# Kernel tuning notes

Measured on AMD Instinct MI355X. Metric: run time of the kernel, lower is better.

## Reference

```python
import jax, jax.numpy as jnp
import numpy as np

B = 4096
P_HID = 1024
H_HID = 512
MAX_P = 128
MAX_HE = MAX_P // 3  # 42
TAU = 1.0
EPS = 1e-20


def setup_inputs() -> dict:
    key = jax.random.key(0)
    ks = jax.random.split(key, 12)
    s_p = 1.0 / np.sqrt(P_HID)
    s_h = 1.0 / np.sqrt(H_HID)
    # gumbel noise: g = -log(-log(U))
    u_p = jax.random.uniform(ks[3], (B, MAX_P, 2), minval=EPS, maxval=1.0)
    u_h = jax.random.uniform(ks[4], (B, MAX_HE, 2), minval=EPS, maxval=1.0)
    return {
        "particle_h": jax.random.normal(ks[0], (B, P_HID), jnp.float32),
        "edge_h": jax.random.normal(ks[1], (B, H_HID), jnp.float32),
        "hyperedge_h": jax.random.normal(ks[2], (B, H_HID), jnp.float32),
        "g_p": -jnp.log(-jnp.log(u_p)),
        "g_h": -jnp.log(-jnp.log(u_h)),
        "W1_p": jax.random.normal(ks[5], (P_HID, P_HID), jnp.float32) * s_p,
        "b1_p": jnp.zeros((P_HID,), jnp.float32),
        "W2_p": jax.random.normal(ks[6], (P_HID, MAX_P), jnp.float32) * s_p,
        "b2_p": jnp.zeros((MAX_P,), jnp.float32),
        "W1_h": jax.random.normal(ks[7], (H_HID, H_HID), jnp.float32) * s_h,
        "b1_h": jnp.zeros((H_HID,), jnp.float32),
        "W2_h": jax.random.normal(ks[8], (H_HID, MAX_HE), jnp.float32) * s_h,
        "b2_h": jnp.zeros((MAX_HE,), jnp.float32),
    }


def _gumbel_hard_st(logits, g, tau):
    """F.gumbel_softmax(stack([l,-l],-1), tau, hard=True)[...,0] (straight-through)."""
    y = jax.nn.softmax((jnp.stack([logits, -logits], axis=-1) + g) / tau, axis=-1)
    y0 = y[..., 0]
    hard0 = (y0 > y[..., 1]).astype(y0.dtype)
    return hard0 + y0 - jax.lax.stop_gradient(y0)


def _mlp(x, W1, b1, W2, b2):
    return jax.nn.gelu(x @ W1 + b1, approximate=False) @ W2 + b2


def reference(particle_h, edge_h, hyperedge_h, g_p, g_h,
              W1_p, b1_p, W2_p, b2_p, W1_h, b1_h, W2_h, b2_h):
    particle_logits = _mlp(particle_h, W1_p, b1_p, W2_p, b2_p)      # [B, MAX_P]
    particle_mask = _gumbel_hard_st(particle_logits, g_p, TAU)      # [B, MAX_P]
    n_particles = particle_mask.sum(axis=-1).astype(jnp.int32)      # [B]

    # Ragged edge lists as a fixed padded buffer: all C(MAX_P,2) lexicographic
    # pairs (same order as torch.combinations); pair (i,j), i<j, is valid for
    # batch b iff j < n_particles[b].
    ii, jj = jnp.triu_indices(MAX_P, k=1)
    edge_index = jnp.stack([ii, jj]).astype(jnp.int32)              # [2, E_max]
    edge_valid = jj[None, :] < n_particles[:, None]                 # [B, E_max] bool

    hyperedge_logits = _mlp(hyperedge_h, W1_h, b1_h, W2_h, b2_h)    # [B, MAX_HE]
    hyperedge_mask = _gumbel_hard_st(hyperedge_logits, g_h, TAU)
    n_hyperedges = hyperedge_mask.sum(axis=-1).astype(jnp.int32)

    return (particle_mask, n_particles, edge_index, edge_valid,
            hyperedge_mask, n_hyperedges)
```

## Files before the change

### kernel.cpp

```cpp
#include <hip/hip_runtime.h>
#include <hip/hip_bf16.h>
#include <math.h>

typedef __bf16 bf16_t;
typedef bf16_t bf16x8 __attribute__((ext_vector_type(8)));
typedef bf16_t bf16x4 __attribute__((ext_vector_type(4)));
typedef float f32x4 __attribute__((ext_vector_type(4)));
typedef unsigned int u32;

#define B_SZ 4096
#define P_HID 1024
#define H_HID 512
#define MAX_P 128
#define MAX_HE 42
#define HE_PAD 64
#define E_MAX 8128
#define E_MAX4 2032

__device__ __forceinline__ void async_cp16(const bf16_t* g, bf16_t* l) {
    __builtin_amdgcn_global_load_lds(
        (const __attribute__((address_space(1))) u32*)g,
        (__attribute__((address_space(3))) u32*)l, 16, 0, 0);
}

__device__ __forceinline__ float gelu_exact(float v) {
    return 0.5f * v * (1.f + erff(v * 0.70710678118654752f));
}

template<int BM, int BN, int MODE>
__global__ __launch_bounds__(256, 2) void gemm_t(
    const bf16_t* __restrict__ Ahi, const bf16_t* __restrict__ Alo,
    const bf16_t* __restrict__ BThi, const bf16_t* __restrict__ BTlo,
    const float* __restrict__ bias,
    bf16_t* __restrict__ Chi, bf16_t* __restrict__ Clo, float* __restrict__ Cf,
    int N, int K, int kchunk)
{
    constexpr int MT = BM / 32;
    constexpr int NT = BN / 32;
    constexpr int OPS_A = BM / 16;
    constexpr int OPS_B = BN / 16;
    constexpr int NOPS = 2 * OPS_A + 2 * OPS_B;

    __shared__ __align__(16) bf16_t smem[(2 * BM + 2 * BN) * 32];
    bf16_t* const As0 = smem;
    bf16_t* const As1 = smem + BM * 32;
    bf16_t* const Bs0 = smem + 2 * BM * 32;
    bf16_t* const Bs1 = smem + 2 * BM * 32 + BN * 32;

    const int tid  = threadIdx.x;
    const int lane = tid & 63;
    const int wid  = tid >> 6;
    const int wm   = wid & 1;
    const int wn   = wid >> 1;
    const int bm   = blockIdx.y * BM;
    const int bn   = blockIdx.x * BN;
    const int k0   = blockIdx.z * kchunk;

    const int srow = lane >> 2;
    const int scol = (lane & 3) * 8;

    f32x4 acc[MT][NT];
#pragma unroll
    for (int i = 0; i < MT; ++i)
#pragma unroll
        for (int j = 0; j < NT; ++j)
            acc[i][j] = (f32x4){0.f, 0.f, 0.f, 0.f};

    const bf16_t* const gA0 = Ahi  + (size_t)bm * K;
    const bf16_t* const gA1 = Alo  + (size_t)bm * K;
    const bf16_t* const gB0 = BThi + (size_t)bn * K;
    const bf16_t* const gB1 = BTlo + (size_t)bn * K;

    const int fr = lane & 15;
    const int fq = lane >> 4;

    for (int kt = k0; kt < k0 + kchunk; kt += 32) {
        __syncthreads();
#pragma unroll
        for (int o = 0; o < NOPS; ++o) {
            if ((o & 3) != wid) continue;
            const bf16_t* gsrc;
            bf16_t* lbase;
            int q;
            if (o < OPS_A)                  { q = o;                     gsrc = gA0; lbase = As0; }
            else if (o < 2 * OPS_A)         { q = o - OPS_A;             gsrc = gA1; lbase = As1; }
            else if (o < 2 * OPS_A + OPS_B) { q = o - 2 * OPS_A;         gsrc = gB0; lbase = Bs0; }
            else                            { q = o - 2 * OPS_A - OPS_B; gsrc = gB1; lbase = Bs1; }
            async_cp16(gsrc + (size_t)(q * 16 + srow) * K + kt + scol,
                       lbase + q * 16 * 32);
        }
        __syncthreads();

        bf16x8 ah[MT], al[MT], bh[NT], bl[NT];
#pragma unroll
        for (int i = 0; i < MT; ++i) {
            const int row = wm * (BM / 2) + i * 16 + fr;
            ah[i] = *(const bf16x8*)(As0 + row * 32 + fq * 8);
            al[i] = *(const bf16x8*)(As1 + row * 32 + fq * 8);
        }
#pragma unroll
        for (int j = 0; j < NT; ++j) {
            const int row = wn * (BN / 2) + j * 16 + fr;
            bh[j] = *(const bf16x8*)(Bs0 + row * 32 + fq * 8);
            bl[j] = *(const bf16x8*)(Bs1 + row * 32 + fq * 8);
        }
#pragma unroll
        for (int i = 0; i < MT; ++i)
#pragma unroll
            for (int j = 0; j < NT; ++j) {
                acc[i][j] = __builtin_amdgcn_mfma_f32_16x16x32_bf16(ah[i], bh[j], acc[i][j], 0, 0, 0);
                acc[i][j] = __builtin_amdgcn_mfma_f32_16x16x32_bf16(ah[i], bl[j], acc[i][j], 0, 0, 0);
                acc[i][j] = __builtin_amdgcn_mfma_f32_16x16x32_bf16(al[i], bh[j], acc[i][j], 0, 0, 0);
            }
    }

#pragma unroll
    for (int i = 0; i < MT; ++i)
#pragma unroll
        for (int j = 0; j < NT; ++j) {
            const int col  = bn + wn * (BN / 2) + j * 16 + fr;
            const int row0 = bm + wm * (BM / 2) + i * 16 + fq * 4;
            if (MODE == 0) {
                const float bj = bias[col];
#pragma unroll
                for (int r = 0; r < 4; ++r) {
                    float v = gelu_exact(acc[i][j][r] + bj);
                    bf16_t h = (bf16_t)v;
                    bf16_t l = (bf16_t)(v - (float)h);
                    const size_t off = (size_t)(row0 + r) * N + col;
                    Chi[off] = h;
                    Clo[off] = l;
                }
            } else {
#pragma unroll
                for (int r = 0; r < 4; ++r)
                    atomicAdd(&Cf[(size_t)(row0 + r) * N + col], acc[i][j][r]);
            }
        }
}

struct PrepArgs {
    const float *ph, *hh, *W1p, *W2p, *W1h, *W2h, *b2p, *b2h;
    bf16_t *pA_hi, *pA_lo, *hA_hi, *hA_lo;
    bf16_t *W1pT_hi, *W1pT_lo, *W2pT_hi, *W2pT_lo;
    bf16_t *W1hT_hi, *W1hT_lo, *W2hT_hi, *W2hT_lo;
    float *log_p, *log_h;
    float *out_ei; int *ws_jj;
};

__device__ __forceinline__ void split4(const float* x, bf16_t* hi, bf16_t* lo, int i) {
    float4 v = ((const float4*)x)[i];
    float vv[4] = {v.x, v.y, v.z, v.w};
    bf16x4 h, l;
#pragma unroll
    for (int r = 0; r < 4; ++r) {
        bf16_t hh = (bf16_t)vv[r];
        h[r] = hh;
        l[r] = (bf16_t)(vv[r] - (float)hh);
    }
    ((bf16x4*)hi)[i] = h;
    ((bf16x4*)lo)[i] = l;
}

__device__ __forceinline__ void tsplit(
    const float* W, bf16_t* Thi, bf16_t* Tlo, int K, int N,
    int t, int nx, float (*sh)[33], int tid)
{
    const int n0 = (t % nx) * 32, k0 = (t / nx) * 32;
    const int tx = tid & 31, ty = tid >> 5;
    for (int r = ty; r < 32; r += 8) {
        const int n = n0 + tx;
        sh[r][tx] = (n < N) ? W[(size_t)(k0 + r) * N + n] : 0.f;
    }
    __syncthreads();
    for (int r = ty; r < 32; r += 8) {
        const float x = sh[tx][r];
        bf16_t h = (bf16_t)x;
        bf16_t l = (bf16_t)(x - (float)h);
        const size_t off = (size_t)(n0 + r) * K + k0 + tx;
        Thi[off] = h;
        Tlo[off] = l;
    }
}

__device__ __forceinline__ int tri_off(int i) { return (i * (255 - i)) >> 1; }

__global__ __launch_bounds__(256) void prep_all(PrepArgs a)
{
    __shared__ float sh[32][33];
    const int bid = blockIdx.x;
    const int tid = threadIdx.x;

    if (bid < 4096) {
        split4(a.ph, a.pA_hi, a.pA_lo, bid * 256 + tid);
    } else if (bid < 6144) {
        split4(a.hh, a.hA_hi, a.hA_lo, (bid - 4096) * 256 + tid);
    } else if (bid < 7168) {
        tsplit(a.W1p, a.W1pT_hi, a.W1pT_lo, P_HID, P_HID, bid - 6144, 32, sh, tid);
    } else if (bid < 7296) {
        tsplit(a.W2p, a.W2pT_hi, a.W2pT_lo, P_HID, MAX_P, bid - 7168, 4, sh, tid);
    } else if (bid < 7552) {
        tsplit(a.W1h, a.W1hT_hi, a.W1hT_lo, H_HID, H_HID, bid - 7296, 16, sh, tid);
    } else if (bid < 7584) {
        tsplit(a.W2h, a.W2hT_hi, a.W2hT_lo, H_HID, MAX_HE, bid - 7552, 2, sh, tid);
    } else if (bid < 7616) {
        const int e = (bid - 7584) * 256 + tid;
        if (e < E_MAX) {
            int i = (int)((255.0 - sqrt(65025.0 - 8.0 * (double)e)) * 0.5);
            if (i < 0) i = 0;
            if (i > 126) i = 126;
            while (i > 0 && tri_off(i) > e) --i;
            while (i < 126 && tri_off(i + 1) <= e) ++i;
            const int j = i + 1 + (e - tri_off(i));
            a.out_ei[e] = (float)i;
            a.out_ei[E_MAX + e] = (float)j;
            a.ws_jj[e] = j;
        }
    } else if (bid < 9664) {
        const int i = (bid - 7616) * 256 + tid;
        a.log_p[i] = a.b2p[i & (MAX_P - 1)];
    } else {
        const int i = (bid - 9664) * 256 + tid;
        const int c = i & (HE_PAD - 1);
        a.log_h[i] = (c < MAX_HE) ? a.b2h[c] : 0.f;
    }
}

__global__ __launch_bounds__(256) void mask_both(
    const float* __restrict__ log_p, const float* __restrict__ g_p,
    const float* __restrict__ log_h, const float* __restrict__ g_h,
    float* __restrict__ out_pmask, float* __restrict__ out_np, int* __restrict__ ws_np,
    float* __restrict__ out_hmask, float* __restrict__ out_nh)
{
    const int gw   = blockIdx.x * 4 + (threadIdx.x >> 6);
    const int lane = threadIdx.x & 63;
    float c = 0.f;
    if (gw < B_SZ) {
        const int row = gw;
#pragma unroll
        for (int h = 0; h < 2; ++h) {
            const int i = lane + 64 * h;
            const size_t idx = (size_t)row * MAX_P + i;
            const float l  = log_p[idx];
            const float g0 = g_p[2 * idx + 0];
            const float g1 = g_p[2 * idx + 1];
            const float m = ((l + g0) > (g1 - l)) ? 1.f : 0.f;
            out_pmask[idx] = m;
            c += m;
        }
#pragma unroll
        for (int off = 32; off > 0; off >>= 1) c += __shfl_xor(c, off, 64);
        if (lane == 0) { out_np[row] = c; ws_np[row] = (int)c; }
    } else {
        const int row = gw - B_SZ;
        if (lane < MAX_HE) {
            const size_t idx = (size_t)row * MAX_HE + lane;
            const float l  = log_h[(size_t)row * HE_PAD + lane];
            const float g0 = g_h[2 * idx + 0];
            const float g1 = g_h[2 * idx + 1];
            const float m = ((l + g0) > (g1 - l)) ? 1.f : 0.f;
            out_hmask[idx] = m;
            c = m;
        }
#pragma unroll
        for (int off = 32; off > 0; off >>= 1) c += __shfl_xor(c, off, 64);
        if (lane == 0) out_nh[row] = c;
    }
}

__global__ __launch_bounds__(256) void edge_valid_kernel(
    const int* __restrict__ ws_jj, const int* __restrict__ ws_n,
    float* __restrict__ out)
{
    const int b   = blockIdx.x >> 1;
    const int seg = blockIdx.x & 1;
    const int n   = ws_n[b];
    const int base = seg * (E_MAX4 / 2);
    float* const orow = out + (size_t)b * E_MAX;
#pragma unroll
    for (int it = 0; it < 4; ++it) {
        const int q = base + it * 256 + threadIdx.x;
        if (q < base + E_MAX4 / 2) {
            const int4 j4 = ((const int4*)ws_jj)[q];
            float4 v;
            v.x = (j4.x < n) ? 1.f : 0.f;
            v.y = (j4.y < n) ? 1.f : 0.f;
            v.z = (j4.z < n) ? 1.f : 0.f;
            v.w = (j4.w < n) ? 1.f : 0.f;
            ((float4*)orow)[q] = v;
        }
    }
}

extern "C" void kernel_launch(void* const* d_in, const int* in_sizes, int n_in,
                              void* d_out, int out_size, void* d_ws, size_t ws_size,
                              hipStream_t stream)
{
    const float* particle_h  = (const float*)d_in[0];
    const float* hyperedge_h = (const float*)d_in[2];
    const float* g_p  = (const float*)d_in[3];
    const float* g_h  = (const float*)d_in[4];
    const float* W1_p = (const float*)d_in[5];
    const float* b1_p = (const float*)d_in[6];
    const float* W2_p = (const float*)d_in[7];
    const float* b2_p = (const float*)d_in[8];
    const float* W1_h = (const float*)d_in[9];
    const float* b1_h = (const float*)d_in[10];
    const float* W2_h = (const float*)d_in[11];
    const float* b2_h = (const float*)d_in[12];

    float* out = (float*)d_out;
    float* out_pmask = out;
    float* out_np    = out_pmask + (size_t)B_SZ * MAX_P;
    float* out_ei    = out_np + B_SZ;
    float* out_ev    = out_ei + 2 * E_MAX;
    float* out_hmask = out_ev + (size_t)B_SZ * E_MAX;
    float* out_nh    = out_hmask + (size_t)B_SZ * MAX_HE;

    char* w = (char*)d_ws;
    bf16_t* pA_hi   = (bf16_t*)w;  w += (size_t)B_SZ * P_HID * 2;
    bf16_t* pA_lo   = (bf16_t*)w;  w += (size_t)B_SZ * P_HID * 2;
    bf16_t* hA_hi   = (bf16_t*)w;  w += (size_t)B_SZ * H_HID * 2;
    bf16_t* hA_lo   = (bf16_t*)w;  w += (size_t)B_SZ * H_HID * 2;
    bf16_t* hidp_hi = (bf16_t*)w;  w += (size_t)B_SZ * P_HID * 2;
    bf16_t* hidp_lo = (bf16_t*)w;  w += (size_t)B_SZ * P_HID * 2;
    bf16_t* hidh_hi = (bf16_t*)w;  w += (size_t)B_SZ * H_HID * 2;
    bf16_t* hidh_lo = (bf16_t*)w;  w += (size_t)B_SZ * H_HID * 2;
    bf16_t* W1pT_hi = (bf16_t*)w;  w += (size_t)P_HID * P_HID * 2;
    bf16_t* W1pT_lo = (bf16_t*)w;  w += (size_t)P_HID * P_HID * 2;
    bf16_t* W2pT_hi = (bf16_t*)w;  w += (size_t)MAX_P * P_HID * 2;
    bf16_t* W2pT_lo = (bf16_t*)w;  w += (size_t)MAX_P * P_HID * 2;
    bf16_t* W1hT_hi = (bf16_t*)w;  w += (size_t)H_HID * H_HID * 2;
    bf16_t* W1hT_lo = (bf16_t*)w;  w += (size_t)H_HID * H_HID * 2;
    bf16_t* W2hT_hi = (bf16_t*)w;  w += (size_t)HE_PAD * H_HID * 2;
    bf16_t* W2hT_lo = (bf16_t*)w;  w += (size_t)HE_PAD * H_HID * 2;
    float*  log_p   = (float*)w;   w += (size_t)B_SZ * MAX_P * 4;
    float*  log_h   = (float*)w;   w += (size_t)B_SZ * HE_PAD * 4;
    int*    ws_np   = (int*)w;     w += B_SZ * 4;
    int*    ws_jj   = (int*)w;

    PrepArgs pa;
    pa.ph = particle_h; pa.hh = hyperedge_h;
    pa.W1p = W1_p; pa.W2p = W2_p; pa.W1h = W1_h; pa.W2h = W2_h;
    pa.b2p = b2_p; pa.b2h = b2_h;
    pa.pA_hi = pA_hi; pa.pA_lo = pA_lo; pa.hA_hi = hA_hi; pa.hA_lo = hA_lo;
    pa.W1pT_hi = W1pT_hi; pa.W1pT_lo = W1pT_lo;
    pa.W2pT_hi = W2pT_hi; pa.W2pT_lo = W2pT_lo;
    pa.W1hT_hi = W1hT_hi; pa.W1hT_lo = W1hT_lo;
    pa.W2hT_hi = W2hT_hi; pa.W2hT_lo = W2hT_lo;
    pa.log_p = log_p; pa.log_h = log_h;
    pa.out_ei = out_ei; pa.ws_jj = ws_jj;
    prep_all<<<10688, 256, 0, stream>>>(pa);

    gemm_t<128, 128, 0><<<dim3(P_HID / 128, B_SZ / 128), 256, 0, stream>>>(
        pA_hi, pA_lo, W1pT_hi, W1pT_lo, b1_p, hidp_hi, hidp_lo, nullptr,
        P_HID, P_HID, P_HID);
    gemm_t<128, 64, 0><<<dim3(H_HID / 64, B_SZ / 128), 256, 0, stream>>>(
        hA_hi, hA_lo, W1hT_hi, W1hT_lo, b1_h, hidh_hi, hidh_lo, nullptr,
        H_HID, H_HID, H_HID);

    gemm_t<128, 128, 1><<<dim3(1, B_SZ / 128, 4), 256, 0, stream>>>(
        hidp_hi, hidp_lo, W2pT_hi, W2pT_lo, nullptr, nullptr, nullptr, log_p,
        MAX_P, P_HID, P_HID / 4);
    gemm_t<128, 64, 1><<<dim3(1, B_SZ / 128, 4), 256, 0, stream>>>(
        hidh_hi, hidh_lo, W2hT_hi, W2hT_lo, nullptr, nullptr, nullptr, log_h,
        HE_PAD, H_HID, H_HID / 4);

    mask_both<<<2 * B_SZ / 4, 256, 0, stream>>>(
        log_p, g_p, log_h, g_h, out_pmask, out_np, ws_np, out_hmask, out_nh);

    edge_valid_kernel<<<2 * B_SZ, 256, 0, stream>>>(ws_jj, ws_np, out_ev);
}
```

Measured before the change: 316.8 us.

## Fuse gumbel mask into second GEMM, load B directly from global, retile

The second-layer GEMMs now apply bias, the Gumbel hard threshold and the per-row count in their epilogue. This removes the split-K atomics, the logits buffers, their bias initialisation in prep, and the separate mask kernel. The B operand is now read straight from global/L2 into registers instead of being staged in LDS. Tile shapes also change: first-layer tiles go to 64x128 and the split-K grids are dropped, so the second layer runs fewer, longer blocks with less parallelism.

```diff
diff --git a/kernel.cpp b/kernel.cpp
--- a/kernel.cpp
+++ b/kernel.cpp
@@ -27,38 +27,38 @@
     return 0.5f * v * (1.f + erff(v * 0.70710678118654752f));
 }
 
-template<int BM, int BN, int MODE>
-__global__ __launch_bounds__(256, 2) void gemm_t(
+template<int BM, int BN, int WM, int WN, int MODE>
+__global__ __launch_bounds__(256, 2) void gemm_f(
     const bf16_t* __restrict__ Ahi, const bf16_t* __restrict__ Alo,
     const bf16_t* __restrict__ BThi, const bf16_t* __restrict__ BTlo,
     const float* __restrict__ bias,
-    bf16_t* __restrict__ Chi, bf16_t* __restrict__ Clo, float* __restrict__ Cf,
-    int N, int K, int kchunk)
-{
-    constexpr int MT = BM / 32;
-    constexpr int NT = BN / 32;
-    constexpr int OPS_A = BM / 16;
-    constexpr int OPS_B = BN / 16;
-    constexpr int NOPS = 2 * OPS_A + 2 * OPS_B;
-
-    __shared__ __align__(16) bf16_t smem[(2 * BM + 2 * BN) * 32];
-    bf16_t* const As0 = smem;
-    bf16_t* const As1 = smem + BM * 32;
-    bf16_t* const Bs0 = smem + 2 * BM * 32;
-    bf16_t* const Bs1 = smem + 2 * BM * 32 + BN * 32;
+    bf16_t* __restrict__ Chi, bf16_t* __restrict__ Clo,
+    int N, int K,
+    const float* __restrict__ g, float* __restrict__ out_mask,
+    float* __restrict__ out_n, int* __restrict__ ws_n, int NV)
+{
+    constexpr int MT = BM / (WM * 16);
+    constexpr int NT = BN / (WN * 16);
+    constexpr int AOPS = BM / 16;
+
+    __shared__ __align__(16) bf16_t As0[BM * 32];
+    __shared__ __align__(16) bf16_t As1[BM * 32];
+    __shared__ float cnt[BM][WN];
 
     const int tid  = threadIdx.x;
     const int lane = tid & 63;
     const int wid  = tid >> 6;
-    const int wm   = wid & 1;
-    const int wn   = wid >> 1;
+    const int wm   = wid % WM;
+    const int wn   = wid / WM;
     const int bm   = blockIdx.y * BM;
     const int bn   = blockIdx.x * BN;
-    const int k0   = blockIdx.z * kchunk;
 
     const int srow = lane >> 2;
     const int scol = (lane & 3) * 8;
 
+    const int fr = lane & 15;
+    const int fq = lane >> 4;
+
     f32x4 acc[MT][NT];
 #pragma unroll
     for (int i = 0; i < MT; ++i)
@@ -66,43 +66,43 @@
         for (int j = 0; j < NT; ++j)
             acc[i][j] = (f32x4){0.f, 0.f, 0.f, 0.f};
 
-    const bf16_t* const gA0 = Ahi  + (size_t)bm * K;
-    const bf16_t* const gA1 = Alo  + (size_t)bm * K;
-    const bf16_t* const gB0 = BThi + (size_t)bn * K;
-    const bf16_t* const gB1 = BTlo + (size_t)bn * K;
-
-    const int fr = lane & 15;
-    const int fq = lane >> 4;
-
-    for (int kt = k0; kt < k0 + kchunk; kt += 32) {
+    const bf16_t* const gA0 = Ahi + (size_t)bm * K;
+    const bf16_t* const gA1 = Alo + (size_t)bm * K;
+    const bf16_t* gBh[NT];
+    const bf16_t* gBl[NT];
+#pragma unroll
+    for (int j = 0; j < NT; ++j) {
+        const size_t row = (size_t)(bn + wn * (BN / WN) + j * 16 + fr);
+        gBh[j] = BThi + row * K + fq * 8;
+        gBl[j] = BTlo + row * K + fq * 8;
+    }
+
+    for (int kt = 0; kt < K; kt += 32) {
         __syncthreads();
 #pragma unroll
-        for (int o = 0; o < NOPS; ++o) {
+        for (int o = 0; o < 2 * AOPS; ++o) {
             if ((o & 3) != wid) continue;
-            const bf16_t* gsrc;
-            bf16_t* lbase;
-            int q;
-            if (o < OPS_A)                  { q = o;                     gsrc = gA0; lbase = As0; }
-            else if (o < 2 * OPS_A)         { q = o - OPS_A;             gsrc = gA1; lbase = As1; }
-            else if (o < 2 * OPS_A + OPS_B) { q = o - 2 * OPS_A;         gsrc = gB0; lbase = Bs0; }
-            else                            { q = o - 2 * OPS_A - OPS_B; gsrc = gB1; lbase = Bs1; }
+            const int plane = o / AOPS;
+            const int q     = o % AOPS;
+            const bf16_t* gsrc = plane ? gA1 : gA0;
+            bf16_t* lbase      = plane ? As1 : As0;
             async_cp16(gsrc + (size_t)(q * 16 + srow) * K + kt + scol,
                        lbase + q * 16 * 32);
         }
+        bf16x8 bh[NT], bl[NT];
+#pragma unroll
+        for (int j = 0; j < NT; ++j) {
+            bh[j] = *(const bf16x8*)(gBh[j] + kt);
+            bl[j] = *(const bf16x8*)(gBl[j] + kt);
+        }
         __syncthreads();
 
-        bf16x8 ah[MT], al[MT], bh[NT], bl[NT];
+        bf16x8 ah[MT], al[MT];
 #pragma unroll
         for (int i = 0; i < MT; ++i) {
-            const int row = wm * (BM / 2) + i * 16 + fr;
+            const int row = wm * (BM / WM) + i * 16 + fr;
             ah[i] = *(const bf16x8*)(As0 + row * 32 + fq * 8);
             al[i] = *(const bf16x8*)(As1 + row * 32 + fq * 8);
-        }
-#pragma unroll
-        for (int j = 0; j < NT; ++j) {
-            const int row = wn * (BN / 2) + j * 16 + fr;
-            bh[j] = *(const bf16x8*)(Bs0 + row * 32 + fq * 8);
-            bl[j] = *(const bf16x8*)(Bs1 + row * 32 + fq * 8);
         }
 #pragma unroll
         for (int i = 0; i < MT; ++i)
@@ -114,13 +114,13 @@
             }
     }
 
-#pragma unroll
-    for (int i = 0; i < MT; ++i)
-#pragma unroll
-        for (int j = 0; j < NT; ++j) {
-            const int col  = bn + wn * (BN / 2) + j * 16 + fr;
-            const int row0 = bm + wm * (BM / 2) + i * 16 + fq * 4;
-            if (MODE == 0) {
+    if (MODE == 0) {
+#pragma unroll
+        for (int i = 0; i < MT; ++i)
+#pragma unroll
+            for (int j = 0; j < NT; ++j) {
+                const int col  = bn + wn * (BN / WN) + j * 16 + fr;
+                const int row0 = bm + wm * (BM / WM) + i * 16 + fq * 4;
                 const float bj = bias[col];
 #pragma unroll
                 for (int r = 0; r < 4; ++r) {
@@ -131,20 +131,51 @@
                     Chi[off] = h;
                     Clo[off] = l;
                 }
-            } else {
-#pragma unroll
-                for (int r = 0; r < 4; ++r)
-                    atomicAdd(&Cf[(size_t)(row0 + r) * N + col], acc[i][j][r]);
             }
-        }
+    } else {
+#pragma unroll
+        for (int i = 0; i < MT; ++i) {
+#pragma unroll
+            for (int r = 0; r < 4; ++r) {
+                const int row_l = wm * (BM / WM) + i * 16 + fq * 4 + r;
+                const int grow  = bm + row_l;
+                float s = 0.f;
+#pragma unroll
+                for (int j = 0; j < NT; ++j) {
+                    const int col = wn * (BN / WN) + j * 16 + fr;
+                    if (col < NV) {
+                        const float v = acc[i][j][r] + bias[col];
+                        const size_t idx = (size_t)grow * NV + col;
+                        const float g0 = g[2 * idx + 0];
+                        const float g1 = g[2 * idx + 1];
+                        const float m = ((v + g0) > (g1 - v)) ? 1.f : 0.f;
+                        out_mask[idx] = m;
+                        s += m;
+                    }
+                }
+                s += __shfl_xor(s, 1, 64);
+                s += __shfl_xor(s, 2, 64);
+                s += __shfl_xor(s, 4, 64);
+                s += __shfl_xor(s, 8, 64);
+                if (fr == 0) cnt[row_l][wn] = s;
+            }
+        }
+        __syncthreads();
+        if (tid < BM) {
+            float c = 0.f;
+#pragma unroll
+            for (int w2 = 0; w2 < WN; ++w2) c += cnt[tid][w2];
+            out_n[bm + tid] = c;
+            if (ws_n) ws_n[bm + tid] = (int)c;
+        }
+    }
 }
 
 struct PrepArgs {
-    const float *ph, *hh, *W1p, *W2p, *W1h, *W2h, *b2p, *b2h;
+    const float *ph, *hh, *W1p, *W2p, *W1h, *W2h;
     bf16_t *pA_hi, *pA_lo, *hA_hi, *hA_lo;
     bf16_t *W1pT_hi, *W1pT_lo, *W2pT_hi, *W2pT_lo;
     bf16_t *W1hT_hi, *W1hT_lo, *W2hT_hi, *W2hT_lo;
-    float *log_p, *log_h;
     float *out_ei; int *ws_jj;
 };
 
@@ -203,7 +234,7 @@
         tsplit(a.W1h, a.W1hT_hi, a.W1hT_lo, H_HID, H_HID, bid - 7296, 16, sh, tid);
     } else if (bid < 7584) {
         tsplit(a.W2h, a.W2hT_hi, a.W2hT_lo, H_HID, MAX_HE, bid - 7552, 2, sh, tid);
-    } else if (bid < 7616) {
+    } else {
         const int e = (bid - 7584) * 256 + tid;
         if (e < E_MAX) {
             int i = (int)((255.0 - sqrt(65025.0 - 8.0 * (double)e)) * 0.5);
@@ -216,55 +247,6 @@
             a.out_ei[E_MAX + e] = (float)j;
             a.ws_jj[e] = j;
         }
-    } else if (bid < 9664) {
-        const int i = (bid - 7616) * 256 + tid;
-        a.log_p[i] = a.b2p[i & (MAX_P - 1)];
-    } else {
-        const int i = (bid - 9664) * 256 + tid;
-        const int c = i & (HE_PAD - 1);
-        a.log_h[i] = (c < MAX_HE) ? a.b2h[c] : 0.f;
-    }
-}
-
-__global__ __launch_bounds__(256) void mask_both(
-    const float* __restrict__ log_p, const float* __restrict__ g_p,
-    const float* __restrict__ log_h, const float* __restrict__ g_h,
-    float* __restrict__ out_pmask, float* __restrict__ out_np, int* __restrict__ ws_np,
-    float* __restrict__ out_hmask, float* __restrict__ out_nh)
-{
-    const int gw   = blockIdx.x * 4 + (threadIdx.x >> 6);
-    const int lane = threadIdx.x & 63;
-    float c = 0.f;
-    if (gw < B_SZ) {
-        const int row = gw;
-#pragma unroll
-        for (int h = 0; h < 2; ++h) {
-            const int i = lane + 64 * h;
-            const size_t idx = (size_t)row * MAX_P + i;
-            const float l  = log_p[idx];
-            const float g0 = g_p[2 * idx + 0];
-            const float g1 = g_p[2 * idx + 1];
-            const float m = ((l + g0) > (g1 - l)) ? 1.f : 0.f;
-            out_pmask[idx] = m;
-            c += m;
-        }
-#pragma unroll
-        for (int off = 32; off > 0; off >>= 1) c += __shfl_xor(c, off, 64);
-        if (lane == 0) { out_np[row] = c; ws_np[row] = (int)c; }
-    } else {
-        const int row = gw - B_SZ;
-        if (lane < MAX_HE) {
-            const size_t idx = (size_t)row * MAX_HE + lane;
-            const float l  = log_h[(size_t)row * HE_PAD + lane];
-            const float g0 = g_h[2 * idx + 0];
-            const float g1 = g_h[2 * idx + 1];
-            const float m = ((l + g0) > (g1 - l)) ? 1.f : 0.f;
-            out_hmask[idx] = m;
-            c = m;
-        }
-#pragma unroll
-        for (int off = 32; off > 0; off >>= 1) c += __shfl_xor(c, off, 64);
-        if (lane == 0) out_nh[row] = c;
     }
 }
 
@@ -334,40 +316,33 @@
     bf16_t* W1hT_lo = (bf16_t*)w;  w += (size_t)H_HID * H_HID * 2;
     bf16_t* W2hT_hi = (bf16_t*)w;  w += (size_t)HE_PAD * H_HID * 2;
     bf16_t* W2hT_lo = (bf16_t*)w;  w += (size_t)HE_PAD * H_HID * 2;
-    float*  log_p   = (float*)w;   w += (size_t)B_SZ * MAX_P * 4;
-    float*  log_h   = (float*)w;   w += (size_t)B_SZ * HE_PAD * 4;
     int*    ws_np   = (int*)w;     w += B_SZ * 4;
     int*    ws_jj   = (int*)w;
 
     PrepArgs pa;
     pa.ph = particle_h; pa.hh = hyperedge_h;
     pa.W1p = W1_p; pa.W2p = W2_p; pa.W1h = W1_h; pa.W2h = W2_h;
-    pa.b2p = b2_p; pa.b2h = b2_h;
     pa.pA_hi = pA_hi; pa.pA_lo = pA_lo; pa.hA_hi = hA_hi; pa.hA_lo = hA_lo;
     pa.W1pT_hi = W1pT_hi; pa.W1pT_lo = W1pT_lo;
     pa.W2pT_hi = W2pT_hi; pa.W2pT_lo = W2pT_lo;
     pa.W1hT_hi = W1hT_hi; pa.W1hT_lo = W1hT_lo;
     pa.W2hT_hi = W2hT_hi; pa.W2hT_lo = W2hT_lo;
-    pa.log_p = log_p; pa.log_h = log_h;
     pa.out_ei = out_ei; pa.ws_jj = ws_jj;
-    prep_all<<<10688, 256, 0, stream>>>(pa);
-
-    gemm_t<128, 128, 0><<<dim3(P_HID / 128, B_SZ / 128), 256, 0, stream>>>(
-        pA_hi, pA_lo, W1pT_hi, W1pT_lo, b1_p, hidp_hi, hidp_lo, nullptr,
-        P_HID, P_HID, P_HID);
-    gemm_t<128, 64, 0><<<dim3(H_HID / 64, B_SZ / 128), 256, 0, stream>>>(
-        hA_hi, hA_lo, W1hT_hi, W1hT_lo, b1_h, hidh_hi, hidh_lo, nullptr,
-        H_HID, H_HID, H_HID);
-
-    gemm_t<128, 128, 1><<<dim3(1, B_SZ / 128, 4), 256, 0, stream>>>(
-        hidp_hi, hidp_lo, W2pT_hi, W2pT_lo, nullptr, nullptr, nullptr, log_p,
-        MAX_P, P_HID, P_HID / 4);
-    gemm_t<128, 64, 1><<<dim3(1, B_SZ / 128, 4), 256, 0, stream>>>(
-        hidh_hi, hidh_lo, W2hT_hi, W2hT_lo, nullptr, nullptr, nullptr, log_h,
-        HE_PAD, H_HID, H_HID / 4);
-
-    mask_both<<<2 * B_SZ / 4, 256, 0, stream>>>(
-        log_p, g_p, log_h, g_h, out_pmask, out_np, ws_np, out_hmask, out_nh);
+    prep_all<<<7616, 256, 0, stream>>>(pa);
+
+    gemm_f<64, 128, 2, 2, 0><<<dim3(P_HID / 128, B_SZ / 64), 256, 0, stream>>>(
+        pA_hi, pA_lo, W1pT_hi, W1pT_lo, b1_p, hidp_hi, hidp_lo,
+        P_HID, P_HID, nullptr, nullptr, nullptr, nullptr, 0);
+    gemm_f<64, 128, 2, 2, 0><<<dim3(H_HID / 128, B_SZ / 64), 256, 0, stream>>>(
+        hA_hi, hA_lo, W1hT_hi, W1hT_lo, b1_h, hidh_hi, hidh_lo,
+        H_HID, H_HID, nullptr, nullptr, nullptr, nullptr, 0);
+
+    gemm_f<32, 128, 1, 4, 1><<<dim3(1, B_SZ / 32), 256, 0, stream>>>(
+        hidp_hi, hidp_lo, W2pT_hi, W2pT_lo, b2_p, nullptr, nullptr,
+        MAX_P, P_HID, g_p, out_pmask, out_np, ws_np, MAX_P);
+    gemm_f<64, 64, 2, 2, 1><<<dim3(1, B_SZ / 64), 256, 0, stream>>>(
+        hidh_hi, hidh_lo, W2hT_hi, W2hT_lo, b2_h, nullptr, nullptr,
+        HE_PAD, H_HID, g_h, out_hmask, out_nh, nullptr, MAX_HE);
 
     edge_valid_kernel<<<2 * B_SZ, 256, 0, stream>>>(ws_jj, ws_np, out_ev);
 }
```

Measured after the change: 361.1 us. +14.0%, slower.
